# Kernel tuning notes

Measured on AMD Instinct MI355X. Metric: run time of the kernel, lower is better.

Reference implementation:

```python
import jax, jax.numpy as jnp
import numpy as np

BS, L, D, H, DC = 8, 8192, 128, 128, 128
C_CONST = 8.0  # rg-lru temperature constant


def _ln(x):
    # LayerNorm without scale/bias (use_bias=False, use_scale=False)
    m = jnp.mean(x, axis=-1, keepdims=True)
    v = jnp.mean(jnp.square(x - m), axis=-1, keepdims=True)
    return (x - m) * jax.lax.rsqrt(v + 1e-6)


def _affine(c, w, b):
    # Dense(features=1)(c)[:, :, None] -> (bs, 1, 1) broadcast scalar per sequence
    return (c @ w + b)[:, :, None]


def _combine(e1, e2):
    a1, b1 = e1
    a2, b2 = e2
    return (a1 * a2, a2 * b1 + b2)


def _linear_scan(a, b, reverse):
    # h_t = a_t * h_{t-1} + b_t (or h_{t+1} when reverse) along seq axis 1
    _, h = jax.lax.associative_scan(_combine, (a, b), axis=1, reverse=reverse)
    return h


def _forward(x, c, cln1_sw, cln1_sb, cln1_bw, cln1_bb, gate1_w, gate1_b,
             rnn_in_w, rnn_in_b, pos_emb, rnn_wi, rnn_bi, rnn_wr, rnn_br, rnn_a,
             rnn_out_w, rnn_out_b, cln2_sw, cln2_sb, cln2_bw, cln2_bb,
             gate2_w, gate2_b, mlp_w1, mlp_b1, mlp_w2, mlp_b2):
    # --- branch 1: conditioned LN -> bidirectional RG-LRU -> gated residual ---
    h = (1.0 + _affine(c, cln1_sw, cln1_sb)) * _ln(x) + _affine(c, cln1_bw, cln1_bb)
    u = _ln(h) @ rnn_in_w + rnn_in_b + pos_emb[None]          # (bs, L, H)
    gi = jax.nn.sigmoid(u @ rnn_wi + rnn_bi)                   # input gate
    gr = jax.nn.sigmoid(u @ rnn_wr + rnn_br)                   # recurrence gate
    at = jnp.exp(C_CONST * gr * jnp.log(rnn_a))                # a_t = a^(c*r_t)
    bt = jnp.sqrt(1.0 - jnp.square(at)) * (gi * u)
    hf = _linear_scan(at, bt, reverse=False)
    hb = _linear_scan(at, bt, reverse=True)
    r = jnp.concatenate([hf, hb], axis=-1) @ rnn_out_w + rnn_out_b  # (bs, L, D)
    x = x + _affine(c, gate1_w, gate1_b) * r
    # --- branch 2: conditioned LN -> gelu MLP -> gated residual ---
    h = (1.0 + _affine(c, cln2_sw, cln2_sb)) * _ln(x) + _affine(c, cln2_bw, cln2_bb)
    m = jax.nn.gelu(h @ mlp_w1 + mlp_b1) @ mlp_w2 + mlp_b2
    return x + _affine(c, gate2_w, gate2_b) * m


def setup_inputs() -> dict:
    key = jax.random.key(0)
    ks = jax.random.split(key, 30)
    def n(k, shape, s=0.05):
        return (jax.random.normal(k, shape) * s).astype(jnp.float32)
    rnn_a = (0.9 + 0.09 * jax.random.uniform(ks[0], (H,))).astype(jnp.float32)
    return {
        "x": jax.random.normal(ks[1], (BS, L, D), jnp.float32),
        "c": jax.random.normal(ks[2], (BS, DC), jnp.float32),
        "cln1_sw": n(ks[3], (DC, 1)), "cln1_sb": n(ks[4], (1,)),
        "cln1_bw": n(ks[5], (DC, 1)), "cln1_bb": n(ks[6], (1,)),
        "gate1_w": n(ks[7], (DC, 1)), "gate1_b": n(ks[8], (1,)),
        "rnn_in_w": n(ks[9], (D, H), 0.1), "rnn_in_b": n(ks[10], (H,)),
        "pos_emb": n(ks[11], (L, H), 0.02),
        "rnn_wi": n(ks[12], (H, H), 0.1), "rnn_bi": n(ks[13], (H,)),
        "rnn_wr": n(ks[14], (H, H), 0.1), "rnn_br": n(ks[15], (H,)),
        "rnn_a": rnn_a,
        "rnn_out_w": n(ks[16], (2 * H, D), 0.1), "rnn_out_b": n(ks[17], (D,)),
        "cln2_sw": n(ks[18], (DC, 1)), "cln2_sb": n(ks[19], (1,)),
        "cln2_bw": n(ks[20], (DC, 1)), "cln2_bb": n(ks[21], (1,)),
        "gate2_w": n(ks[22], (DC, 1)), "gate2_b": n(ks[23], (1,)),
        "mlp_w1": n(ks[24], (D, 4 * D), 0.1), "mlp_b1": n(ks[25], (4 * D,)),
        "mlp_w2": n(ks[26], (4 * D, D), 0.1), "mlp_b2": n(ks[27], (D,)),
    }


def reference(x, c, cln1_sw, cln1_sb, cln1_bw, cln1_bb, gate1_w, gate1_b,
              rnn_in_w, rnn_in_b, pos_emb, rnn_wi, rnn_bi, rnn_wr, rnn_br, rnn_a,
              rnn_out_w, rnn_out_b, cln2_sw, cln2_sb, cln2_bw, cln2_bb,
              gate2_w, gate2_b, mlp_w1, mlp_b1, mlp_w2, mlp_b2):
    return _forward(x, c, cln1_sw, cln1_sb, cln1_bw, cln1_bb, gate1_w, gate1_b,
                    rnn_in_w, rnn_in_b, pos_emb, rnn_wi, rnn_bi, rnn_wr, rnn_br, rnn_a,
                    rnn_out_w, rnn_out_b, cln2_sw, cln2_sb, cln2_bw, cln2_bb,
                    gate2_w, gate2_b, mlp_w1, mlp_b1, mlp_w2, mlp_b2)
```

## Files before the change

kernel.cpp:

```cpp
#include <hip/hip_runtime.h>
#include <hip/hip_bf16.h>

#define BSZ 8
#define SEQ 8192
#define DIM 128
#define NCH 128
#define CLEN 64

typedef unsigned short u16;
typedef unsigned int u32;
typedef short bf16x8 __attribute__((ext_vector_type(8)));
typedef float f32x4  __attribute__((ext_vector_type(4)));

__device__ __forceinline__ float us2f(u16 w){ union{u32 i;float f;}u; u.i=((u32)w)<<16; return u.f; }
__device__ __forceinline__ u16 f2us(float f){
  __hip_bfloat16 h = __float2bfloat16(f);
  union{ __hip_bfloat16 b; u16 s; }u; u.b=h; return u.s;
}
__device__ __forceinline__ float wred64(float v){
  #pragma unroll
  for (int o=1;o<64;o<<=1) v += __shfl_xor(v,o,64);
  return v;
}
__device__ __forceinline__ float red16(float v){
  v += __shfl_xor(v,1,64); v += __shfl_xor(v,2,64);
  v += __shfl_xor(v,4,64); v += __shfl_xor(v,8,64);
  return v;
}
__device__ __forceinline__ float sigmoidf_(float z){ return 1.f/(1.f+__expf(-z)); }
__device__ __forceinline__ float gelu_tanh(float x){
  float y = 0.7978845608028654f * fmaf(0.044715f*x, x*x, x);
  float e = __expf(2.f*y);
  float th = 1.f - 2.f/(e+1.f);
  return 0.5f*x*(1.f+th);
}

__global__ __launch_bounds__(64) void k_aff(
    const float* __restrict__ c,
    const float* w0,const float* w1,const float* w2,const float* w3,const float* w4,const float* w5,
    const float* s0,const float* s1,const float* s2,const float* s3,const float* s4,const float* s5,
    float* __restrict__ aff)
{
  const float* ws[6]={w0,w1,w2,w3,w4,w5};
  const float* bs[6]={s0,s1,s2,s3,s4,s5};
  int l = threadIdx.x;
  for (int b=0;b<BSZ;++b){
    #pragma unroll
    for (int h=0;h<6;++h){
      float v = c[b*128+l]*ws[h][l] + c[b*128+64+l]*ws[h][64+l];
      v = wred64(v);
      if (l==0) aff[b*6+h] = v + bs[h][0];
    }
  }
}

__global__ __launch_bounds__(256) void k_prep(
    const float* __restrict__ w1, const float* __restrict__ w2, const float* __restrict__ wo,
    const float* __restrict__ win, const float* __restrict__ wi, const float* __restrict__ wr,
    u16* __restrict__ w1t, u16* __restrict__ w2t, u16* __restrict__ wot,
    u16* __restrict__ wint, u16* __restrict__ wit, u16* __restrict__ wrt)
{
  int i = blockIdx.x*256 + threadIdx.x;
  { int n=i>>7, k=i&127; w1t[i] = f2us(w1[k*512+n]); }
  { int n=i>>9, k=i&511; w2t[i] = f2us(w2[k*128+n]); }
  if (i < 32768){ int n=i>>8, k=i&255; wot[i] = f2us(wo[k*128+n]); }
  if (i < 16384){
    int n=i>>7, k=i&127;
    wint[i] = f2us(win[k*128+n]);
    wit[i]  = f2us(wi[k*128+n]);
    wrt[i]  = f2us(wr[k*128+n]);
  }
}

__global__ __launch_bounds__(256,2) void k_pre(
    const float* __restrict__ xg, const u16* __restrict__ wint, const float* __restrict__ b_in,
    const float* __restrict__ pos, const u16* __restrict__ wit, const float* __restrict__ b_i,
    const u16* __restrict__ wrt, const float* __restrict__ b_r, const float* __restrict__ avec,
    const float* __restrict__ aff,
    u16* __restrict__ atg, u16* __restrict__ btg,
    float* __restrict__ Ag, float* __restrict__ Bfg, float* __restrict__ Bbg)
{
  __shared__ u16 A_l[CLEN*136];
  __shared__ u16 wT[128*72];
  __shared__ u32 abp[CLEN*DIM];
  const int t  = threadIdx.x;
  const int b  = blockIdx.x >> 7;
  const int ck = blockIdx.x & (NCH-1);
  const size_t base = ((size_t)(b*SEQ + ck*CLEN))*DIM;
  const int lane=t&63, wv=t>>6, col=lane&15, quad=lane>>4;
  const int m0 = wv*16;

  {
    const float s1p = 1.f + aff[b*6+0];
    const int ln = t&63;
    for (int i=0;i<16;++i){
      int r = wv*16 + i;
      float2 v = *(const float2*)(xg + base + (size_t)r*DIM + 2*ln);
      float m  = wred64(v.x+v.y)*(1.f/128.f);
      float d0=v.x-m, d1=v.y-m;
      float var = wred64(d0*d0+d1*d1)*(1.f/128.f);
      float rs = rsqrtf(var + 1e-6f);
      float vz = var*rs*rs;
      float tt2 = s1p*rsqrtf(fmaf(s1p*s1p, vz, 1e-6f));
      float sc = rs*tt2;
      u32 pk = (u32)f2us(d0*sc) | ((u32)f2us(d1*sc)<<16);
      *(u32*)&A_l[r*136 + 2*ln] = pk;
    }
  }

  f32x4 uacc[8];
  #pragma unroll
  for (int n=0;n<8;++n) uacc[n]=(f32x4){0.f,0.f,0.f,0.f};
  for (int c=0;c<2;++c){
    __syncthreads();
    for (int i=t;i<1024;i+=256){
      int n=i>>3, cc=(i&7)*8;
      *(uint4*)&wT[n*72+cc] = *(const uint4*)&wint[(size_t)n*128 + c*64 + cc];
    }
    __syncthreads();
    #pragma unroll
    for (int k2=0;k2<2;++k2){
      bf16x8 av = *(const bf16x8*)&A_l[(m0+col)*136 + c*64 + k2*32 + quad*8];
      #pragma unroll
      for (int n=0;n<8;++n){
        bf16x8 bv = *(const bf16x8*)&wT[(n*16+col)*72 + k2*32 + quad*8];
        uacc[n] = __builtin_amdgcn_mfma_f32_16x16x32_bf16(av, bv, uacc[n], 0,0,0);
      }
    }
  }
  float u_c[8][4];
  #pragma unroll
  for (int n=0;n<8;++n){
    int nc = n*16 + col;
    float bi = b_in[nc];
    #pragma unroll
    for (int r=0;r<4;++r){
      int row = m0 + quad*4 + r;
      u_c[n][r] = uacc[n][r] + bi + pos[(size_t)(ck*CLEN+row)*DIM + nc];
    }
  }
  __syncthreads();

  #pragma unroll
  for (int n=0;n<8;++n){
    #pragma unroll
    for (int r=0;r<4;++r)
      A_l[(m0+quad*4+r)*136 + n*16+col] = f2us(u_c[n][r]);
  }

  f32x4 gacc[8];
  #pragma unroll
  for (int n=0;n<8;++n) gacc[n]=(f32x4){0.f,0.f,0.f,0.f};
  for (int c=0;c<2;++c){
    __syncthreads();
    for (int i=t;i<1024;i+=256){
      int n=i>>3, cc=(i&7)*8;
      *(uint4*)&wT[n*72+cc] = *(const uint4*)&wit[(size_t)n*128 + c*64 + cc];
    }
    __syncthreads();
    #pragma unroll
    for (int k2=0;k2<2;++k2){
      bf16x8 av = *(const bf16x8*)&A_l[(m0+col)*136 + c*64 + k2*32 + quad*8];
      #pragma unroll
      for (int n=0;n<8;++n){
        bf16x8 bv = *(const bf16x8*)&wT[(n*16+col)*72 + k2*32 + quad*8];
        gacc[n] = __builtin_amdgcn_mfma_f32_16x16x32_bf16(av, bv, gacc[n], 0,0,0);
      }
    }
  }
  float gi_c[8][4];
  #pragma unroll
  for (int n=0;n<8;++n){
    float bi = b_i[n*16+col];
    #pragma unroll
    for (int r=0;r<4;++r) gi_c[n][r] = sigmoidf_(gacc[n][r]+bi);
  }

  f32x4 racc[8];
  #pragma unroll
  for (int n=0;n<8;++n) racc[n]=(f32x4){0.f,0.f,0.f,0.f};
  for (int c=0;c<2;++c){
    __syncthreads();
    for (int i=t;i<1024;i+=256){
      int n=i>>3, cc=(i&7)*8;
      *(uint4*)&wT[n*72+cc] = *(const uint4*)&wrt[(size_t)n*128 + c*64 + cc];
    }
    __syncthreads();
    #pragma unroll
    for (int k2=0;k2<2;++k2){
      bf16x8 av = *(const bf16x8*)&A_l[(m0+col)*136 + c*64 + k2*32 + quad*8];
      #pragma unroll
      for (int n=0;n<8;++n){
        bf16x8 bv = *(const bf16x8*)&wT[(n*16+col)*72 + k2*32 + quad*8];
        racc[n] = __builtin_amdgcn_mfma_f32_16x16x32_bf16(av, bv, racc[n], 0,0,0);
      }
    }
  }

  #pragma unroll
  for (int n=0;n<8;++n){
    int nc = n*16 + col;
    float la = __logf(avec[nc]);
    float br = b_r[nc];
    #pragma unroll
    for (int r=0;r<4;++r){
      int row = m0 + quad*4 + r;
      float g = sigmoidf_(racc[n][r]+br);
      float a = __expf(8.f*g*la);
      float bb = sqrtf(fmaxf(1.f-a*a,0.f))*gi_c[n][r]*u_c[n][r];
      u16 ab_ = f2us(a), bb_ = f2us(bb);
      abp[row*DIM+nc] = (u32)ab_ | ((u32)bb_<<16);
      atg[base + (size_t)row*DIM + nc] = ab_;
      btg[base + (size_t)row*DIM + nc] = bb_;
    }
  }
  __syncthreads();

  const int sbase = (b*NCH+ck)*DIM;
  if (t < 128){
    float h=0.f, p=1.f;
    #pragma unroll 4
    for (int tt=0;tt<CLEN;++tt){
      u32 v=abp[tt*DIM+t];
      float a=us2f((u16)v), bb=us2f((u16)(v>>16));
      h=fmaf(a,h,bb); p*=a;
    }
    Ag[sbase+t]=p; Bfg[sbase+t]=h;
  } else {
    int ch=t-128; float h=0.f;
    #pragma unroll 4
    for (int tt=CLEN-1;tt>=0;--tt){
      u32 v=abp[tt*DIM+ch];
      h=fmaf(us2f((u16)v),h,us2f((u16)(v>>16)));
    }
    Bbg[sbase+ch]=h;
  }
}

__global__ __launch_bounds__(128) void k_chunkscan(
    const float* __restrict__ Ag, const float* __restrict__ Bfg, const float* __restrict__ Bbg,
    float* __restrict__ Hf, float* __restrict__ Hb)
{
  const int dir = blockIdx.x >> 3, b = blockIdx.x & 7, ch = threadIdx.x;
  float s = 0.f;
  if (dir==0){
    for (int c=0;c<NCH;++c){ size_t i=((size_t)(b*NCH+c))*DIM+ch; Hf[i]=s; s=fmaf(Ag[i],s,Bfg[i]); }
  } else {
    for (int c=NCH-1;c>=0;--c){ size_t i=((size_t)(b*NCH+c))*DIM+ch; Hb[i]=s; s=fmaf(Ag[i],s,Bbg[i]); }
  }
}

__global__ __launch_bounds__(256,2) void k_scan(
    const u16* __restrict__ atg, const u16* __restrict__ btg,
    const float* __restrict__ Hf, const float* __restrict__ Hb,
    const float* __restrict__ xg, const u16* __restrict__ wot, const float* __restrict__ b_out,
    const float* __restrict__ aff, float* __restrict__ outg)
{
  __shared__ u16 sm[CLEN*DIM*2];
  __shared__ u16 hcat[CLEN*264];
  u16* a_l = sm;
  u16* b_l = sm + CLEN*DIM;
  const int t  = threadIdx.x;
  const int b  = blockIdx.x >> 7;
  const int ck = blockIdx.x & (NCH-1);
  const size_t base = ((size_t)(b*SEQ + ck*CLEN))*DIM;

  {
    const uint4* sa=(const uint4*)(atg+base); const uint4* sb=(const uint4*)(btg+base);
    for (int i=t;i<1024;i+=256){ ((uint4*)a_l)[i]=sa[i]; ((uint4*)b_l)[i]=sb[i]; }
  }
  __syncthreads();

  const int pbase=(b*NCH+ck)*DIM;
  if (t<128){
    float h=Hf[pbase+t];
    #pragma unroll 4
    for (int tt=0;tt<CLEN;++tt){
      h=fmaf(us2f(a_l[tt*DIM+t]),h,us2f(b_l[tt*DIM+t]));
      hcat[tt*264+t]=f2us(h);
    }
  } else {
    int ch=t-128;
    float h=Hb[pbase+ch];
    #pragma unroll 4
    for (int tt=CLEN-1;tt>=0;--tt){
      h=fmaf(us2f(a_l[tt*DIM+ch]),h,us2f(b_l[tt*DIM+ch]));
      hcat[tt*264+128+ch]=f2us(h);
    }
  }
  __syncthreads();

  const int lane=t&63, wv=t>>6, col=lane&15, quad=lane>>4;
  const int m0 = wv*16;
  u16* wol = sm;
  f32x4 acc[8];
  #pragma unroll
  for (int n=0;n<8;++n) acc[n]=(f32x4){0.f,0.f,0.f,0.f};
  for (int chk=0; chk<4; ++chk){
    for (int i=t;i<1024;i+=256){
      int n=i>>3, c=(i&7)*8;
      *(uint4*)&wol[n*72 + c] = *(const uint4*)&wot[(size_t)n*256 + chk*64 + c];
    }
    __syncthreads();
    #pragma unroll
    for (int k2=0;k2<2;++k2){
      bf16x8 av = *(const bf16x8*)&hcat[(m0+col)*264 + chk*64 + k2*32 + quad*8];
      #pragma unroll
      for (int n=0;n<8;++n){
        bf16x8 bv = *(const bf16x8*)&wol[(n*16+col)*72 + k2*32 + quad*8];
        acc[n] = __builtin_amdgcn_mfma_f32_16x16x32_bf16(av, bv, acc[n], 0,0,0);
      }
    }
    __syncthreads();
  }
  const float g1=aff[b*6+2];
  #pragma unroll
  for (int n=0;n<8;++n){
    int nc = n*16 + col;
    float bo = b_out[nc];
    #pragma unroll
    for (int r=0;r<4;++r){
      int row = m0 + quad*4 + r;
      size_t gi = base + (size_t)row*DIM + nc;
      outg[gi] = fmaf(g1, acc[n][r]+bo, xg[gi]);
    }
  }
}

__global__ __launch_bounds__(256,3) void k_mlp(
    const u16* __restrict__ w1t, const float* __restrict__ b1v,
    const u16* __restrict__ w2t, const float* __restrict__ b2v,
    const float* __restrict__ aff, float* __restrict__ outg)
{
  __shared__ u16 h2l[CLEN*136];
  __shared__ u16 wbuf[128*72];
  __shared__ u16 m1p[CLEN*136];
  const int t=threadIdx.x;
  const int b=blockIdx.x>>7;
  const size_t base=(size_t)blockIdx.x*CLEN*DIM;
  const int lane=t&63, wv=t>>6, col=lane&15, quad=lane>>4;
  const int m0 = wv*16;
  const float s2p=1.f+aff[b*6+3], b2a=aff[b*6+4], g2=aff[b*6+5];

  {
    const int cg=t&15, rg=t>>4, j0=cg*8, r0=rg*4;
    #pragma unroll
    for (int ii=0;ii<4;++ii){
      int r=r0+ii;
      const float* xo = outg + base + (size_t)r*DIM + j0;
      float4 a = *(const float4*)xo;
      float4 bq = *(const float4*)(xo+4);
      float o[8]={a.x,a.y,a.z,a.w,bq.x,bq.y,bq.z,bq.w};
      float s=0.f;
      #pragma unroll
      for (int j=0;j<8;++j) s+=o[j];
      s=red16(s); float m=s*(1.f/128.f);
      float q2=0.f;
      #pragma unroll
      for (int j=0;j<8;++j){ float d=o[j]-m; q2+=d*d; }
      q2=red16(q2); float rs=rsqrtf(q2*(1.f/128.f)+1e-6f);
      u32 pk[4];
      #pragma unroll
      for (int q=0;q<4;++q){
        float a0=fmaf((o[2*q]-m)*rs,   s2p, b2a);
        float a1=fmaf((o[2*q+1]-m)*rs, s2p, b2a);
        pk[q]= (u32)f2us(a0) | ((u32)f2us(a1)<<16);
      }
      *(uint4*)&h2l[r*136+j0] = make_uint4(pk[0],pk[1],pk[2],pk[3]);
    }
  }

  f32x4 acc2[8];
  #pragma unroll
  for (int n=0;n<8;++n) acc2[n]=(f32x4){0.f,0.f,0.f,0.f};

  for (int p=0;p<4;++p){
    f32x4 accp[8];
    #pragma unroll
    for (int n=0;n<8;++n) accp[n]=(f32x4){0.f,0.f,0.f,0.f};
    for (int c=0;c<2;++c){
      __syncthreads();
      for (int i=t;i<1024;i+=256){
        int n=i>>3, cc=(i&7)*8;
        *(uint4*)&wbuf[n*72+cc] = *(const uint4*)&w1t[(size_t)(p*128+n)*128 + c*64 + cc];
      }
      __syncthreads();
      #pragma unroll
      for (int k2=0;k2<2;++k2){
        bf16x8 av = *(const bf16x8*)&h2l[(m0+col)*136 + c*64 + k2*32 + quad*8];
        #pragma unroll
        for (int n=0;n<8;++n){
          bf16x8 bv = *(const bf16x8*)&wbuf[(n*16+col)*72 + k2*32 + quad*8];
          accp[n] = __builtin_amdgcn_mfma_f32_16x16x32_bf16(av, bv, accp[n], 0,0,0);
        }
      }
    }
    #pragma unroll
    for (int n=0;n<8;++n){
      int nc = n*16 + col;
      float bb = b1v[p*128 + nc];
      #pragma unroll
      for (int r=0;r<4;++r)
        m1p[(m0+quad*4+r)*136 + nc] = f2us(gelu_tanh(accp[n][r] + bb));
    }
    for (int c=0;c<2;++c){
      __syncthreads();
      for (int i=t;i<1024;i+=256){
        int n=i>>3, cc=(i&7)*8;
        *(uint4*)&wbuf[n*72+cc] = *(const uint4*)&w2t[(size_t)n*512 + p*128 + c*64 + cc];
      }
      __syncthreads();
      #pragma unroll
      for (int k2=0;k2<2;++k2){
        bf16x8 av = *(const bf16x8*)&m1p[(m0+col)*136 + c*64 + k2*32 + quad*8];
        #pragma unroll
        for (int n=0;n<8;++n){
          bf16x8 bv = *(const bf16x8*)&wbuf[(n*16+col)*72 + k2*32 + quad*8];
          acc2[n] = __builtin_amdgcn_mfma_f32_16x16x32_bf16(av, bv, acc2[n], 0,0,0);
        }
      }
    }
  }
  #pragma unroll
  for (int n=0;n<8;++n){
    int nc = n*16 + col;
    float bb = b2v[nc];
    #pragma unroll
    for (int r=0;r<4;++r){
      int row = m0 + quad*4 + r;
      size_t gi = base + (size_t)row*DIM + nc;
      outg[gi] = fmaf(g2, acc2[n][r] + bb, outg[gi]);
    }
  }
}

extern "C" void kernel_launch(void* const* d_in, const int* in_sizes, int n_in,
                              void* d_out, int out_size, void* d_ws, size_t ws_size,
                              hipStream_t stream)
{
  (void)in_sizes; (void)n_in; (void)out_size; (void)ws_size;
  const float* x   =(const float*)d_in[0];
  const float* c   =(const float*)d_in[1];
  const float* c1sw=(const float*)d_in[2];  const float* c1sb=(const float*)d_in[3];
  const float* c1bw=(const float*)d_in[4];  const float* c1bb=(const float*)d_in[5];
  const float* g1w =(const float*)d_in[6];  const float* g1b =(const float*)d_in[7];
  const float* win =(const float*)d_in[8];  const float* binv=(const float*)d_in[9];
  const float* pos =(const float*)d_in[10];
  const float* wi  =(const float*)d_in[11]; const float* biv =(const float*)d_in[12];
  const float* wr  =(const float*)d_in[13]; const float* brv =(const float*)d_in[14];
  const float* av  =(const float*)d_in[15];
  const float* wout=(const float*)d_in[16]; const float* bout=(const float*)d_in[17];
  const float* c2sw=(const float*)d_in[18]; const float* c2sb=(const float*)d_in[19];
  const float* c2bw=(const float*)d_in[20]; const float* c2bb=(const float*)d_in[21];
  const float* g2w =(const float*)d_in[22]; const float* g2b =(const float*)d_in[23];
  const float* w1  =(const float*)d_in[24]; const float* b1v =(const float*)d_in[25];
  const float* w2  =(const float*)d_in[26]; const float* b2v =(const float*)d_in[27];

  float* wsf  = (float*)d_ws;
  float* Ag   = wsf;
  float* Bfg  = Ag   + 131072;
  float* Bbg  = Bfg  + 131072;
  float* Hf   = Bbg  + 131072;
  float* Hb   = Hf   + 131072;
  float* aff  = Hb   + 131072;
  u16*   w1t  = (u16*)(aff + 64);
  u16*   w2t  = w1t + 65536;
  u16*   wot  = w2t + 65536;
  u16*   wint = wot + 32768;
  u16*   wit  = wint + 16384;
  u16*   wrt  = wit  + 16384;
  u16*   atg  = wrt  + 16384;
  u16*   btg  = atg  + 8388608;

  float* outg = (float*)d_out;

  k_aff<<<dim3(1),dim3(64),0,stream>>>(c, c1sw,c1bw,g1w,c2sw,c2bw,g2w,
                                       c1sb,c1bb,g1b,c2sb,c2bb,g2b, aff);
  k_prep<<<dim3(256),dim3(256),0,stream>>>(w1,w2,wout,win,wi,wr,
                                           w1t,w2t,wot,wint,wit,wrt);
  k_pre<<<dim3(BSZ*NCH),dim3(256),0,stream>>>(x,wint,binv,pos,wit,biv,wrt,brv,av,aff,
                                              atg,btg, Ag,Bfg,Bbg);
  k_chunkscan<<<dim3(16),dim3(128),0,stream>>>(Ag,Bfg,Bbg,Hf,Hb);
  k_scan<<<dim3(BSZ*NCH),dim3(256),0,stream>>>(atg,btg,Hf,Hb,x,wot,bout,aff,outg);
  k_mlp<<<dim3(BSZ*NCH),dim3(256),0,stream>>>(w1t,b1v,w2t,b2v,aff,outg);
}
```

Measured before the change: 329.7 us.

## Fuse scan and MLP kernels, pack a/b, read weights directly from global

Merges the affine-conditioning kernel into the weight-prep kernel and fuses the scan/output-projection kernel with the MLP kernel. The intermediate x1 now stays in registers instead of round-tripping through the output buffer. The a_t and b_t values are packed into one u32 array, and the scan reads it straight from global memory instead of staging it in LDS. All MFMA B-operand weight staging through LDS is dropped in favour of direct global/L2 reads, which cuts LDS use and barriers so occupancy can be raised to 3 blocks. The tradeoff is more uncoalesced global traffic for weight fragments and for the per-timestep scan loads.

```diff
diff --git a/kernel.cpp b/kernel.cpp
--- a/kernel.cpp
+++ b/kernel.cpp
@@ -35,32 +35,34 @@
   return 0.5f*x*(1.f+th);
 }
 
-__global__ __launch_bounds__(64) void k_aff(
+__global__ __launch_bounds__(256) void k_prep(
     const float* __restrict__ c,
-    const float* w0,const float* w1,const float* w2,const float* w3,const float* w4,const float* w5,
+    const float* a0,const float* a1,const float* a2,const float* a3,const float* a4,const float* a5,
     const float* s0,const float* s1,const float* s2,const float* s3,const float* s4,const float* s5,
-    float* __restrict__ aff)
-{
-  const float* ws[6]={w0,w1,w2,w3,w4,w5};
-  const float* bs[6]={s0,s1,s2,s3,s4,s5};
-  int l = threadIdx.x;
-  for (int b=0;b<BSZ;++b){
-    #pragma unroll
-    for (int h=0;h<6;++h){
-      float v = c[b*128+l]*ws[h][l] + c[b*128+64+l]*ws[h][64+l];
-      v = wred64(v);
-      if (l==0) aff[b*6+h] = v + bs[h][0];
-    }
-  }
-}
-
-__global__ __launch_bounds__(256) void k_prep(
     const float* __restrict__ w1, const float* __restrict__ w2, const float* __restrict__ wo,
     const float* __restrict__ win, const float* __restrict__ wi, const float* __restrict__ wr,
     u16* __restrict__ w1t, u16* __restrict__ w2t, u16* __restrict__ wot,
-    u16* __restrict__ wint, u16* __restrict__ wit, u16* __restrict__ wrt)
+    u16* __restrict__ wint, u16* __restrict__ wit, u16* __restrict__ wrt,
+    float* __restrict__ aff)
 {
-  int i = blockIdx.x*256 + threadIdx.x;
+  const int bx = blockIdx.x;
+  if (bx == 256){
+    if (threadIdx.x < 64){
+      const float* ws[6]={a0,a1,a2,a3,a4,a5};
+      const float* bs[6]={s0,s1,s2,s3,s4,s5};
+      int l = threadIdx.x;
+      for (int b=0;b<BSZ;++b){
+        #pragma unroll
+        for (int h=0;h<6;++h){
+          float v = c[b*128+l]*ws[h][l] + c[b*128+64+l]*ws[h][64+l];
+          v = wred64(v);
+          if (l==0) aff[b*6+h] = v + bs[h][0];
+        }
+      }
+    }
+    return;
+  }
+  int i = bx*256 + threadIdx.x;
   { int n=i>>7, k=i&127; w1t[i] = f2us(w1[k*512+n]); }
   { int n=i>>9, k=i&511; w2t[i] = f2us(w2[k*128+n]); }
   if (i < 32768){ int n=i>>8, k=i&255; wot[i] = f2us(wo[k*128+n]); }
@@ -72,17 +74,16 @@
   }
 }
 
-__global__ __launch_bounds__(256,2) void k_pre(
+__global__ __launch_bounds__(256,3) void k_pre(
     const float* __restrict__ xg, const u16* __restrict__ wint, const float* __restrict__ b_in,
     const float* __restrict__ pos, const u16* __restrict__ wit, const float* __restrict__ b_i,
     const u16* __restrict__ wrt, const float* __restrict__ b_r, const float* __restrict__ avec,
     const float* __restrict__ aff,
-    u16* __restrict__ atg, u16* __restrict__ btg,
+    u32* __restrict__ abg,
     float* __restrict__ Ag, float* __restrict__ Bfg, float* __restrict__ Bbg)
 {
   __shared__ u16 A_l[CLEN*136];
-  __shared__ u16 wT[128*72];
-  __shared__ u32 abp[CLEN*DIM];
+  __shared__ u32 abp[CLEN*132];
   const int t  = threadIdx.x;
   const int b  = blockIdx.x >> 7;
   const int ck = blockIdx.x & (NCH-1);
@@ -92,9 +93,9 @@
 
   {
     const float s1p = 1.f + aff[b*6+0];
-    const int ln = t&63;
+    const int ln = lane;
     for (int i=0;i<16;++i){
-      int r = wv*16 + i;
+      int r = m0 + i;
       float2 v = *(const float2*)(xg + base + (size_t)r*DIM + 2*ln);
       float m  = wred64(v.x+v.y)*(1.f/128.f);
       float d0=v.x-m, d1=v.y-m;
@@ -103,27 +104,22 @@
       float vz = var*rs*rs;
       float tt2 = s1p*rsqrtf(fmaf(s1p*s1p, vz, 1e-6f));
       float sc = rs*tt2;
-      u32 pk = (u32)f2us(d0*sc) | ((u32)f2us(d1*sc)<<16);
-      *(u32*)&A_l[r*136 + 2*ln] = pk;
-    }
-  }
+      *(u32*)&A_l[r*136 + 2*ln] = (u32)f2us(d0*sc) | ((u32)f2us(d1*sc)<<16);
+    }
+  }
+  __syncthreads();
 
   f32x4 uacc[8];
   #pragma unroll
   for (int n=0;n<8;++n) uacc[n]=(f32x4){0.f,0.f,0.f,0.f};
+  #pragma unroll
   for (int c=0;c<2;++c){
-    __syncthreads();
-    for (int i=t;i<1024;i+=256){
-      int n=i>>3, cc=(i&7)*8;
-      *(uint4*)&wT[n*72+cc] = *(const uint4*)&wint[(size_t)n*128 + c*64 + cc];
-    }
-    __syncthreads();
     #pragma unroll
     for (int k2=0;k2<2;++k2){
       bf16x8 av = *(const bf16x8*)&A_l[(m0+col)*136 + c*64 + k2*32 + quad*8];
       #pragma unroll
       for (int n=0;n<8;++n){
-        bf16x8 bv = *(const bf16x8*)&wT[(n*16+col)*72 + k2*32 + quad*8];
+        bf16x8 bv = *(const bf16x8*)&wint[(size_t)(n*16+col)*128 + c*64 + k2*32 + quad*8];
         uacc[n] = __builtin_amdgcn_mfma_f32_16x16x32_bf16(av, bv, uacc[n], 0,0,0);
       }
     }
@@ -147,23 +143,19 @@
     for (int r=0;r<4;++r)
       A_l[(m0+quad*4+r)*136 + n*16+col] = f2us(u_c[n][r]);
   }
+  __syncthreads();
 
   f32x4 gacc[8];
   #pragma unroll
   for (int n=0;n<8;++n) gacc[n]=(f32x4){0.f,0.f,0.f,0.f};
+  #pragma unroll
   for (int c=0;c<2;++c){
-    __syncthreads();
-    for (int i=t;i<1024;i+=256){
-      int n=i>>3, cc=(i&7)*8;
-      *(uint4*)&wT[n*72+cc] = *(const uint4*)&wit[(size_t)n*128 + c*64 + cc];
-    }
-    __syncthreads();
     #pragma unroll
     for (int k2=0;k2<2;++k2){
       bf16x8 av = *(const bf16x8*)&A_l[(m0+col)*136 + c*64 + k2*32 + quad*8];
       #pragma unroll
       for (int n=0;n<8;++n){
-        bf16x8 bv = *(const bf16x8*)&wT[(n*16+col)*72 + k2*32 + quad*8];
+        bf16x8 bv = *(const bf16x8*)&wit[(size_t)(n*16+col)*128 + c*64 + k2*32 + quad*8];
         gacc[n] = __builtin_amdgcn_mfma_f32_16x16x32_bf16(av, bv, gacc[n], 0,0,0);
       }
     }
@@ -179,19 +171,14 @@
   f32x4 racc[8];
   #pragma unroll
   for (int n=0;n<8;++n) racc[n]=(f32x4){0.f,0.f,0.f,0.f};
+  #pragma unroll
   for (int c=0;c<2;++c){
-    __syncthreads();
-    for (int i=t;i<1024;i+=256){
-      int n=i>>3, cc=(i&7)*8;
-      *(uint4*)&wT[n*72+cc] = *(const uint4*)&wrt[(size_t)n*128 + c*64 + cc];
-    }
-    __syncthreads();
     #pragma unroll
     for (int k2=0;k2<2;++k2){
       bf16x8 av = *(const bf16x8*)&A_l[(m0+col)*136 + c*64 + k2*32 + quad*8];
       #pragma unroll
       for (int n=0;n<8;++n){
-        bf16x8 bv = *(const bf16x8*)&wT[(n*16+col)*72 + k2*32 + quad*8];
+        bf16x8 bv = *(const bf16x8*)&wrt[(size_t)(n*16+col)*128 + c*64 + k2*32 + quad*8];
         racc[n] = __builtin_amdgcn_mfma_f32_16x16x32_bf16(av, bv, racc[n], 0,0,0);
       }
     }
@@ -208,10 +195,9 @@
       float g = sigmoidf_(racc[n][r]+br);
       float a = __expf(8.f*g*la);
       float bb = sqrtf(fmaxf(1.f-a*a,0.f))*gi_c[n][r]*u_c[n][r];
-      u16 ab_ = f2us(a), bb_ = f2us(bb);
-      abp[row*DIM+nc] = (u32)ab_ | ((u32)bb_<<16);
-      atg[base + (size_t)row*DIM + nc] = ab_;
-      btg[base + (size_t)row*DIM + nc] = bb_;
+      u32 pk = (u32)f2us(a) | ((u32)f2us(bb)<<16);
+      abp[row*132+nc] = pk;
+      abg[base + (size_t)row*DIM + nc] = pk;
     }
   }
   __syncthreads();
@@ -221,7 +207,7 @@
     float h=0.f, p=1.f;
     #pragma unroll 4
     for (int tt=0;tt<CLEN;++tt){
-      u32 v=abp[tt*DIM+t];
+      u32 v=abp[tt*132+t];
       float a=us2f((u16)v), bb=us2f((u16)(v>>16));
       h=fmaf(a,h,bb); p*=a;
     }
@@ -230,7 +216,7 @@
     int ch=t-128; float h=0.f;
     #pragma unroll 4
     for (int tt=CLEN-1;tt>=0;--tt){
-      u32 v=abp[tt*DIM+ch];
+      u32 v=abp[tt*132+ch];
       h=fmaf(us2f((u16)v),h,us2f((u16)(v>>16)));
     }
     Bbg[sbase+ch]=h;
@@ -250,33 +236,31 @@
   }
 }
 
-__global__ __launch_bounds__(256,2) void k_scan(
-    const u16* __restrict__ atg, const u16* __restrict__ btg,
-    const float* __restrict__ Hf, const float* __restrict__ Hb,
+__global__ __launch_bounds__(256,3) void k_scanmlp(
+    const u32* __restrict__ abg, const float* __restrict__ Hf, const float* __restrict__ Hb,
     const float* __restrict__ xg, const u16* __restrict__ wot, const float* __restrict__ b_out,
+    const u16* __restrict__ w1t, const float* __restrict__ b1v,
+    const u16* __restrict__ w2t, const float* __restrict__ b2v,
     const float* __restrict__ aff, float* __restrict__ outg)
 {
-  __shared__ u16 sm[CLEN*DIM*2];
-  __shared__ u16 hcat[CLEN*264];
-  u16* a_l = sm;
-  u16* b_l = sm + CLEN*DIM;
+  __shared__ u16 ubuf[2*CLEN*136];
+  u16* hcat = ubuf;
+  u16* h2l  = ubuf;
+  u16* m1p  = ubuf + CLEN*136;
   const int t  = threadIdx.x;
   const int b  = blockIdx.x >> 7;
   const int ck = blockIdx.x & (NCH-1);
   const size_t base = ((size_t)(b*SEQ + ck*CLEN))*DIM;
-
-  {
-    const uint4* sa=(const uint4*)(atg+base); const uint4* sb=(const uint4*)(btg+base);
-    for (int i=t;i<1024;i+=256){ ((uint4*)a_l)[i]=sa[i]; ((uint4*)b_l)[i]=sb[i]; }
-  }
-  __syncthreads();
+  const int lane=t&63, wv=t>>6, col=lane&15, quad=lane>>4;
+  const int m0 = wv*16;
 
   const int pbase=(b*NCH+ck)*DIM;
   if (t<128){
     float h=Hf[pbase+t];
     #pragma unroll 4
     for (int tt=0;tt<CLEN;++tt){
-      h=fmaf(us2f(a_l[tt*DIM+t]),h,us2f(b_l[tt*DIM+t]));
+      u32 v = abg[base + (size_t)tt*DIM + t];
+      h=fmaf(us2f((u16)v),h,us2f((u16)(v>>16)));
       hcat[tt*264+t]=f2us(h);
     }
   } else {
@@ -284,36 +268,30 @@
     float h=Hb[pbase+ch];
     #pragma unroll 4
     for (int tt=CLEN-1;tt>=0;--tt){
-      h=fmaf(us2f(a_l[tt*DIM+ch]),h,us2f(b_l[tt*DIM+ch]));
+      u32 v = abg[base + (size_t)tt*DIM + ch];
+      h=fmaf(us2f((u16)v),h,us2f((u16)(v>>16)));
       hcat[tt*264+128+ch]=f2us(h);
     }
   }
   __syncthreads();
 
-  const int lane=t&63, wv=t>>6, col=lane&15, quad=lane>>4;
-  const int m0 = wv*16;
-  u16* wol = sm;
   f32x4 acc[8];
   #pragma unroll
   for (int n=0;n<8;++n) acc[n]=(f32x4){0.f,0.f,0.f,0.f};
+  #pragma unroll
   for (int chk=0; chk<4; ++chk){
-    for (int i=t;i<1024;i+=256){
-      int n=i>>3, c=(i&7)*8;
-      *(uint4*)&wol[n*72 + c] = *(const uint4*)&wot[(size_t)n*256 + chk*64 + c];
-    }
-    __syncthreads();
     #pragma unroll
     for (int k2=0;k2<2;++k2){
       bf16x8 av = *(const bf16x8*)&hcat[(m0+col)*264 + chk*64 + k2*32 + quad*8];
       #pragma unroll
       for (int n=0;n<8;++n){
-        bf16x8 bv = *(const bf16x8*)&wol[(n*16+col)*72 + k2*32 + quad*8];
+        bf16x8 bv = *(const bf16x8*)&wot[(size_t)(n*16+col)*256 + chk*64 + k2*32 + quad*8];
         acc[n] = __builtin_amdgcn_mfma_f32_16x16x32_bf16(av, bv, acc[n], 0,0,0);
       }
     }
-    __syncthreads();
   }
   const float g1=aff[b*6+2];
+  float x1r[8][4];
   #pragma unroll
   for (int n=0;n<8;++n){
     int nc = n*16 + col;
@@ -321,80 +299,48 @@
     #pragma unroll
     for (int r=0;r<4;++r){
       int row = m0 + quad*4 + r;
-      size_t gi = base + (size_t)row*DIM + nc;
-      outg[gi] = fmaf(g1, acc[n][r]+bo, xg[gi]);
-    }
-  }
-}
-
-__global__ __launch_bounds__(256,3) void k_mlp(
-    const u16* __restrict__ w1t, const float* __restrict__ b1v,
-    const u16* __restrict__ w2t, const float* __restrict__ b2v,
-    const float* __restrict__ aff, float* __restrict__ outg)
-{
-  __shared__ u16 h2l[CLEN*136];
-  __shared__ u16 wbuf[128*72];
-  __shared__ u16 m1p[CLEN*136];
-  const int t=threadIdx.x;
-  const int b=blockIdx.x>>7;
-  const size_t base=(size_t)blockIdx.x*CLEN*DIM;
-  const int lane=t&63, wv=t>>6, col=lane&15, quad=lane>>4;
-  const int m0 = wv*16;
+      x1r[n][r] = fmaf(g1, acc[n][r]+bo, xg[base + (size_t)row*DIM + nc]);
+    }
+  }
+  __syncthreads();
+
   const float s2p=1.f+aff[b*6+3], b2a=aff[b*6+4], g2=aff[b*6+5];
-
-  {
-    const int cg=t&15, rg=t>>4, j0=cg*8, r0=rg*4;
-    #pragma unroll
-    for (int ii=0;ii<4;++ii){
-      int r=r0+ii;
-      const float* xo = outg + base + (size_t)r*DIM + j0;
-      float4 a = *(const float4*)xo;
-      float4 bq = *(const float4*)(xo+4);
-      float o[8]={a.x,a.y,a.z,a.w,bq.x,bq.y,bq.z,bq.w};
-      float s=0.f;
-      #pragma unroll
-      for (int j=0;j<8;++j) s+=o[j];
-      s=red16(s); float m=s*(1.f/128.f);
-      float q2=0.f;
-      #pragma unroll
-      for (int j=0;j<8;++j){ float d=o[j]-m; q2+=d*d; }
-      q2=red16(q2); float rs=rsqrtf(q2*(1.f/128.f)+1e-6f);
-      u32 pk[4];
-      #pragma unroll
-      for (int q=0;q<4;++q){
-        float a0=fmaf((o[2*q]-m)*rs,   s2p, b2a);
-        float a1=fmaf((o[2*q+1]-m)*rs, s2p, b2a);
-        pk[q]= (u32)f2us(a0) | ((u32)f2us(a1)<<16);
-      }
-      *(uint4*)&h2l[r*136+j0] = make_uint4(pk[0],pk[1],pk[2],pk[3]);
-    }
-  }
+  #pragma unroll
+  for (int r=0;r<4;++r){
+    float s=0.f;
+    #pragma unroll
+    for (int n=0;n<8;++n) s+=x1r[n][r];
+    s=red16(s); float m=s*(1.f/128.f);
+    float q2=0.f;
+    #pragma unroll
+    for (int n=0;n<8;++n){ float d=x1r[n][r]-m; q2+=d*d; }
+    q2=red16(q2); float rs=rsqrtf(q2*(1.f/128.f)+1e-6f);
+    #pragma unroll
+    for (int n=0;n<8;++n)
+      h2l[(m0+quad*4+r)*136 + n*16+col] = f2us(fmaf((x1r[n][r]-m)*rs, s2p, b2a));
+  }
+  __syncthreads();
 
   f32x4 acc2[8];
   #pragma unroll
   for (int n=0;n<8;++n) acc2[n]=(f32x4){0.f,0.f,0.f,0.f};
-
   for (int p=0;p<4;++p){
     f32x4 accp[8];
     #pragma unroll
     for (int n=0;n<8;++n) accp[n]=(f32x4){0.f,0.f,0.f,0.f};
+    #pragma unroll
     for (int c=0;c<2;++c){
-      __syncthreads();
-      for (int i=t;i<1024;i+=256){
-        int n=i>>3, cc=(i&7)*8;
-        *(uint4*)&wbuf[n*72+cc] = *(const uint4*)&w1t[(size_t)(p*128+n)*128 + c*64 + cc];
-      }
-      __syncthreads();
       #pragma unroll
       for (int k2=0;k2<2;++k2){
         bf16x8 av = *(const bf16x8*)&h2l[(m0+col)*136 + c*64 + k2*32 + quad*8];
         #pragma unroll
         for (int n=0;n<8;++n){
-          bf16x8 bv = *(const bf16x8*)&wbuf[(n*16+col)*72 + k2*32 + quad*8];
+          bf16x8 bv = *(const bf16x8*)&w1t[(size_t)(p*128+n*16+col)*128 + c*64 + k2*32 + quad*8];
           accp[n] = __builtin_amdgcn_mfma_f32_16x16x32_bf16(av, bv, accp[n], 0,0,0);
         }
       }
     }
+    __syncthreads();
     #pragma unroll
     for (int n=0;n<8;++n){
       int nc = n*16 + col;
@@ -403,19 +349,15 @@
       for (int r=0;r<4;++r)
         m1p[(m0+quad*4+r)*136 + nc] = f2us(gelu_tanh(accp[n][r] + bb));
     }
+    __syncthreads();
+    #pragma unroll
     for (int c=0;c<2;++c){
-      __syncthreads();
-      for (int i=t;i<1024;i+=256){
-        int n=i>>3, cc=(i&7)*8;
-        *(uint4*)&wbuf[n*72+cc] = *(const uint4*)&w2t[(size_t)n*512 + p*128 + c*64 + cc];
-      }
-      __syncthreads();
       #pragma unroll
       for (int k2=0;k2<2;++k2){
         bf16x8 av = *(const bf16x8*)&m1p[(m0+col)*136 + c*64 + k2*32 + quad*8];
         #pragma unroll
         for (int n=0;n<8;++n){
-          bf16x8 bv = *(const bf16x8*)&wbuf[(n*16+col)*72 + k2*32 + quad*8];
+          bf16x8 bv = *(const bf16x8*)&w2t[(size_t)(n*16+col)*512 + p*128 + c*64 + k2*32 + quad*8];
           acc2[n] = __builtin_amdgcn_mfma_f32_16x16x32_bf16(av, bv, acc2[n], 0,0,0);
         }
       }
@@ -428,8 +370,7 @@
     #pragma unroll
     for (int r=0;r<4;++r){
       int row = m0 + quad*4 + r;
-      size_t gi = base + (size_t)row*DIM + nc;
-      outg[gi] = fmaf(g2, acc2[n][r] + bb, outg[gi]);
+      outg[base + (size_t)row*DIM + nc] = fmaf(g2, acc2[n][r] + bb, x1r[n][r]);
     }
   }
 }
@@ -469,18 +410,17 @@
   u16*   wint = wot + 32768;
   u16*   wit  = wint + 16384;
   u16*   wrt  = wit  + 16384;
-  u16*   atg  = wrt  + 16384;
-  u16*   btg  = atg  + 8388608;
+  u32*   abg  = (u32*)(wrt + 16384);
 
   float* outg = (float*)d_out;
 
-  k_aff<<<dim3(1),dim3(64),0,stream>>>(c, c1sw,c1bw,g1w,c2sw,c2bw,g2w,
-                                       c1sb,c1bb,g1b,c2sb,c2bb,g2b, aff);
-  k_prep<<<dim3(256),dim3(256),0,stream>>>(w1,w2,wout,win,wi,wr,
-                                           w1t,w2t,wot,wint,wit,wrt);
+  k_prep<<<dim3(257),dim3(256),0,stream>>>(c, c1sw,c1bw,g1w,c2sw,c2bw,g2w,
+                                           c1sb,c1bb,g1b,c2sb,c2bb,g2b,
+                                           w1,w2,wout,win,wi,wr,
+                                           w1t,w2t,wot,wint,wit,wrt, aff);
   k_pre<<<dim3(BSZ*NCH),dim3(256),0,stream>>>(x,wint,binv,pos,wit,biv,wrt,brv,av,aff,
-                                              atg,btg, Ag,Bfg,Bbg);
+                                              abg, Ag,Bfg,Bbg);
   k_chunkscan<<<dim3(16),dim3(128),0,stream>>>(Ag,Bfg,Bbg,Hf,Hb);
-  k_scan<<<dim3(BSZ*NCH),dim3(256),0,stream>>>(atg,btg,Hf,Hb,x,wot,bout,aff,outg);
-  k_mlp<<<dim3(BSZ*NCH),dim3(256),0,stream>>>(w1t,b1v,w2t,b2v,aff,outg);
-}
+  k_scanmlp<<<dim3(BSZ*NCH),dim3(256),0,stream>>>(abg,Hf,Hb,x,wot,bout,
+                                                  w1t,b1v,w2t,b2v,aff,outg);
+}
```

New measurement: 449.6 us. 1.36x slower.
